# Kernel tuning notes

Measured on AMD Instinct MI355X. Metric: run time of the kernel, lower is better.

The kernel has to match this reference:

```python
import jax, jax.numpy as jnp
import numpy as np

EMB = 64
N_LEFT = 100000   # m: rows of left_features, b
N_RIGHT = 100000  # n: rows of right_features, c
N_EDGES = 3200000


def setup_inputs() -> dict:
    key = jax.random.key(0)
    ks = jax.random.split(key, 12)
    inp = {
        "left_features": jax.random.normal(ks[0], (N_LEFT, EMB), jnp.float32),
        "right_features_k": jax.random.normal(ks[1], (N_RIGHT, EMB), jnp.float32),
        "edge_index": jax.random.randint(ks[2], (N_EDGES, 2), 0, N_RIGHT, jnp.int64),
        "edge_weight": jax.random.uniform(ks[3], (N_EDGES,), jnp.float32),
        "right_features": jax.random.normal(ks[4], (N_RIGHT, EMB), jnp.float32),
        "c": jax.random.normal(ks[5], (N_RIGHT, 1), jnp.float32),
        "b": jax.random.normal(ks[6], (N_LEFT, 1), jnp.float32),
        # learned parameters
        "temp": jnp.full((2,), 0.9, jnp.float32),
        "W1": jax.random.normal(ks[7], (EMB, EMB), jnp.float32) * 0.05,
        "b1": jnp.zeros((EMB,), jnp.float32),
        "W2": jax.random.normal(ks[8], (EMB, EMB), jnp.float32) * 0.05,
        "b2": jnp.zeros((EMB,), jnp.float32),
    }
    return inp


def reference(left_features, right_features_k, edge_index, edge_weight,
              right_features, c, b, temp, W1, b1, W2, b2):
    # right_to_left=False branch of BipartiteGraphConvolution.forward
    n = right_features.shape[0]  # = c.shape[0]
    # Source quirk: values.sum(dim=-1) on a 1-D vector is a GLOBAL scalar sum,
    # clamped to min 1; every edge weight is scaled by 1/that scalar.
    total = jnp.maximum(jnp.sum(edge_weight), 1.0)
    vals = edge_weight / total                                    # [E]
    row = edge_index[:, 0]  # destination (right) node, in [0, n)
    col = edge_index[:, 1]  # source (left) node, in [0, m)
    # sparse-dense matmul: conv_output = A @ left_features, A in COO (coalesce
    # just sums duplicate entries, identical to segment-sum over raw edges)
    msg = left_features[col] * vals[:, None]                      # [E, EMB]
    conv_output = jax.ops.segment_sum(msg, row, num_segments=n)   # [n, EMB]
    h = right_features + temp[1] * (c - conv_output)              # [n, EMB]
    # output_module: Linear -> ReLU -> Linear (torch Linear: x @ W.T + b)
    h = jax.nn.relu(h @ W1.T + b1)
    out = h @ W2.T + b2
    return out
```

## Files before the change

### kernel.cpp

```cpp
#include <hip/hip_runtime.h>

#define EMB 64
#define BROWS 512
#define BSHIFT 9
#define CHUNK2 2048
#define COLBITS 23
#define COLMASK ((1u << COLBITS) - 1u)
#define MROWS 64
#define HPAD 66

__device__ __forceinline__ unsigned short f2bf(float f) {
    unsigned u = __float_as_uint(f);
    u = u + 0x7FFFu + ((u >> 16) & 1u);
    return (unsigned short)(u >> 16);
}

__global__ void convert_left_kernel(const float* __restrict__ left,
                                    unsigned* __restrict__ left16, int n2) {
    int i = blockIdx.x * blockDim.x + threadIdx.x;
    if (i >= n2) return;
    float2 v = ((const float2*)left)[i];
    left16[i] = (unsigned)f2bf(v.x) | ((unsigned)f2bf(v.y) << 16);
}

__global__ void init_bcur_kernel(int* __restrict__ bcur, int nb, int slot) {
    int t = threadIdx.x;
    if (t < nb) bcur[t] = t * slot;
}

__global__ __launch_bounds__(256) void partition2_kernel(
    const int2* __restrict__ eidx, const float* __restrict__ w, int n_edges,
    int nb, int* __restrict__ bcursor, int2* __restrict__ bsorted,
    float* __restrict__ total) {
    __shared__ int lcur[256];
    __shared__ int go[256];
    int t = threadIdx.x;
    int base = blockIdx.x * CHUNK2;

    lcur[t] = 0;
    __syncthreads();

    int2 pay[8];
    int bb[8];
    int rr[8];
    float s = 0.f;
    #pragma unroll
    for (int k = 0; k < 8; ++k) {
        int e = base + t + k * 256;
        if (e < n_edges) {
            int2 rc = eidx[e];
            float wv = w[e];
            s += wv;
            int b = rc.x >> BSHIFT;
            pay[k] = make_int2(
                (int)(((unsigned)(rc.x & (BROWS - 1)) << COLBITS) |
                      (unsigned)rc.y),
                __float_as_int(wv));
            bb[k] = b;
            rr[k] = atomicAdd(&lcur[b], 1);
        } else {
            bb[k] = -1;
        }
    }
    #pragma unroll
    for (int off = 32; off > 0; off >>= 1) s += __shfl_down(s, off, 64);
    if ((t & 63) == 0) atomicAdd(total, s);
    __syncthreads();

    if (t < nb) {
        int v = lcur[t];
        go[t] = (v > 0) ? atomicAdd(&bcursor[t], v) : 0;
    }
    __syncthreads();

    #pragma unroll
    for (int k = 0; k < 8; ++k) {
        if (bb[k] >= 0) bsorted[(size_t)go[bb[k]] + rr[k]] = pay[k];
    }
}

__global__ __launch_bounds__(256, 1) void count_scan_kernel(
    const int* __restrict__ bcur, int* __restrict__ sbase, int nb, int slot) {
    __shared__ int ssc[256];
    int t = threadIdx.x;
    int cnt = (t < nb) ? (bcur[t] - t * slot) : 0;
    ssc[t] = cnt;
    __syncthreads();
    for (int off = 1; off < 256; off <<= 1) {
        int u = (t >= off) ? ssc[t - off] : 0;
        __syncthreads();
        ssc[t] += u;
        __syncthreads();
    }
    if (t < nb) sbase[t] = ssc[t] - cnt;
}

__global__ __launch_bounds__(1024) void local_rowsort_kernel(
    const int2* __restrict__ bsorted, const int* __restrict__ bcur,
    const int* __restrict__ sbase, int* __restrict__ offs,
    int2* __restrict__ sorted2, int n_right, int slot) {
    __shared__ int lhist[BROWS];
    __shared__ int lcur[BROWS];
    __shared__ int ps[BROWS];
    int b = blockIdx.x;
    int t = threadIdx.x;
    int src0 = b * slot;
    int send = min(bcur[b], src0 + slot);
    int dbase = sbase[b];
    int row0 = b << BSHIFT;
    int nrows = min(BROWS, n_right - row0);

    if (t < BROWS) lhist[t] = 0;
    __syncthreads();
    for (int e = src0 + t; e < send; e += 1024)
        atomicAdd(&lhist[((unsigned)bsorted[e].x) >> COLBITS], 1);
    __syncthreads();

    if (t < BROWS) ps[t] = lhist[t];
    __syncthreads();
    for (int off = 1; off < BROWS; off <<= 1) {
        int u = (t < BROWS && t >= off) ? ps[t - off] : 0;
        __syncthreads();
        if (t < BROWS) ps[t] += u;
        __syncthreads();
    }
    if (t < BROWS) {
        int excl = ps[t] - lhist[t];
        lcur[t] = excl;
        if (t < nrows) offs[row0 + t] = dbase + excl;
    }
    __syncthreads();

    int e = src0 + t;
    for (; e + 3 * 1024 < send; e += 4 * 1024) {
        int2 e0 = bsorted[e + 0 * 1024];
        int2 e1 = bsorted[e + 1 * 1024];
        int2 e2 = bsorted[e + 2 * 1024];
        int2 e3 = bsorted[e + 3 * 1024];
        int p0 = atomicAdd(&lcur[((unsigned)e0.x) >> COLBITS], 1);
        int p1 = atomicAdd(&lcur[((unsigned)e1.x) >> COLBITS], 1);
        int p2 = atomicAdd(&lcur[((unsigned)e2.x) >> COLBITS], 1);
        int p3 = atomicAdd(&lcur[((unsigned)e3.x) >> COLBITS], 1);
        sorted2[dbase + p0] = e0;
        sorted2[dbase + p1] = e1;
        sorted2[dbase + p2] = e2;
        sorted2[dbase + p3] = e3;
    }
    for (; e < send; e += 1024) {
        int2 e0 = bsorted[e];
        int p0 = atomicAdd(&lcur[((unsigned)e0.x) >> COLBITS], 1);
        sorted2[dbase + p0] = e0;
    }
}

__global__ void seg_gather_bf16_kernel(const int2* __restrict__ sorted,
                                       const int* __restrict__ offs,
                                       const uint4* __restrict__ left16o,
                                       const float* __restrict__ right,
                                       const float* __restrict__ c,
                                       const float* __restrict__ temp,
                                       const float* __restrict__ total,
                                       float* __restrict__ hout, int n_right,
                                       int n_edges, int offs_are_ends) {
    int gid = blockIdx.x * blockDim.x + threadIdx.x;
    int wid = gid >> 6;
    int lane = gid & 63;
    if (wid >= n_right) return;
    int start, end;
    if (offs_are_ends) {
        end = offs[wid];
        start = (wid == 0) ? 0 : offs[wid - 1];
    } else {
        start = offs[wid];
        end = (wid + 1 < n_right) ? offs[wid + 1] : n_edges;
    }

    int sub = lane >> 3;
    int d8  = lane & 7;

    float cv = c[wid];
    float inv = 1.0f / fmaxf(total[0], 1.0f);
    float t1 = temp[1];

    float a0 = 0.f, a1 = 0.f, a2 = 0.f, a3 = 0.f;
    float a4 = 0.f, a5 = 0.f, a6 = 0.f, a7 = 0.f;

    if (start < end) {
        int ee = start + sub;
        int2 sv = sorted[(ee < end) ? ee : (end - 1)];
        for (int base = start; base < end; base += 8) {
            int2 cur = sv;
            int ecur = base + sub;
            int bnext = base + 8;
            if (bnext < end) {
                int en = bnext + sub;
                sv = sorted[(en < end) ? en : (end - 1)];
            }
            float wv = (ecur < end) ? __int_as_float(cur.y) : 0.f;
            unsigned col = (unsigned)cur.x & COLMASK;
            uint4 pk = left16o[(size_t)col * 8 + d8];
            a0 = fmaf(wv, __uint_as_float(pk.x << 16), a0);
            a1 = fmaf(wv, __uint_as_float(pk.x & 0xffff0000u), a1);
            a2 = fmaf(wv, __uint_as_float(pk.y << 16), a2);
            a3 = fmaf(wv, __uint_as_float(pk.y & 0xffff0000u), a3);
            a4 = fmaf(wv, __uint_as_float(pk.z << 16), a4);
            a5 = fmaf(wv, __uint_as_float(pk.z & 0xffff0000u), a5);
            a6 = fmaf(wv, __uint_as_float(pk.w << 16), a6);
            a7 = fmaf(wv, __uint_as_float(pk.w & 0xffff0000u), a7);
        }
    }

    #define RED8(x) x += __shfl_xor(x, 8, 64); x += __shfl_xor(x, 16, 64); \
                    x += __shfl_xor(x, 32, 64);
    RED8(a0) RED8(a1) RED8(a2) RED8(a3) RED8(a4) RED8(a5) RED8(a6) RED8(a7)
    #undef RED8

    if (lane < 8) {
        const float4* rp = (const float4*)(right + (size_t)wid * EMB);
        float4 r0 = rp[2 * lane];
        float4 r1 = rp[2 * lane + 1];
        float4 h0, h1;
        h0.x = r0.x + t1 * (cv - a0 * inv);
        h0.y = r0.y + t1 * (cv - a1 * inv);
        h0.z = r0.z + t1 * (cv - a2 * inv);
        h0.w = r0.w + t1 * (cv - a3 * inv);
        h1.x = r1.x + t1 * (cv - a4 * inv);
        h1.y = r1.y + t1 * (cv - a5 * inv);
        h1.z = r1.z + t1 * (cv - a6 * inv);
        h1.w = r1.w + t1 * (cv - a7 * inv);
        float4* op = (float4*)(hout + (size_t)wid * EMB);
        op[2 * lane] = h0;
        op[2 * lane + 1] = h1;
    }
}

__global__ __launch_bounds__(256, 4) void mlp_kernel(
    const float* __restrict__ W1, const float* __restrict__ b1,
    const float* __restrict__ W2, const float* __restrict__ b2,
    float* __restrict__ io, int n) {
    __shared__ float hT[64 * HPAD];
    __shared__ float h1T[64 * 64];
    int t = threadIdx.x;
    int r = t & 63;
    int q = __builtin_amdgcn_readfirstlane(t >> 6);
    int row0 = blockIdx.x * MROWS;

    #pragma unroll
    for (int i = 0; i < 16; ++i) {
        int rr = i * 4 + q;
        int gr = row0 + rr;
        float v = (gr < n) ? io[(size_t)gr * EMB + r] : 0.f;
        hT[r * HPAD + rr] = v;
    }
    __syncthreads();

    float acc[16];
    #pragma unroll
    for (int jj = 0; jj < 16; ++jj) acc[jj] = b1[q * 16 + jj];
    for (int k = 0; k < 64; ++k) {
        float hk = hT[k * HPAD + r];
        #pragma unroll
        for (int jj = 0; jj < 16; ++jj)
            acc[jj] = fmaf(hk, W1[(q * 16 + jj) * EMB + k], acc[jj]);
    }
    #pragma unroll
    for (int jj = 0; jj < 16; ++jj)
        h1T[(q * 16 + jj) * 64 + r] = fmaxf(acc[jj], 0.f);
    __syncthreads();

    #pragma unroll
    for (int jj = 0; jj < 16; ++jj) acc[jj] = b2[q * 16 + jj];
    for (int k = 0; k < 64; ++k) {
        float hk = h1T[k * 64 + r];
        #pragma unroll
        for (int jj = 0; jj < 16; ++jj)
            acc[jj] = fmaf(hk, W2[(q * 16 + jj) * EMB + k], acc[jj]);
    }
    __syncthreads();
    #pragma unroll
    for (int jj = 0; jj < 16; ++jj)
        hT[(q * 16 + jj) * HPAD + r] = acc[jj];
    __syncthreads();

    #pragma unroll
    for (int i = 0; i < 16; ++i) {
        int rr = i * 4 + q;
        int gr = row0 + rr;
        if (gr < n) io[(size_t)gr * EMB + r] = hT[r * HPAD + rr];
    }
}


__global__ void hist_total_kernel(const int2* __restrict__ eidx,
                                  const float* __restrict__ w, int n_edges,
                                  int* __restrict__ counts,
                                  float* __restrict__ total) {
    int gid = blockIdx.x * blockDim.x + threadIdx.x;
    int stride = gridDim.x * blockDim.x;
    float s = 0.f;
    for (int e = gid; e < n_edges; e += stride) {
        s += w[e];
        atomicAdd(&counts[eidx[e].x], 1);
    }
    #pragma unroll
    for (int off = 32; off > 0; off >>= 1) s += __shfl_down(s, off, 64);
    if ((threadIdx.x & 63) == 0) atomicAdd(total, s);
}

__global__ __launch_bounds__(1024, 1) void scan1_kernel(
    const int* __restrict__ cnt, int* __restrict__ incl,
    int* __restrict__ bsums, int n) {
    __shared__ int s[1024];
    int t = threadIdx.x;
    int i = blockIdx.x * 1024 + t;
    int v = (i < n) ? cnt[i] : 0;
    s[t] = v;
    __syncthreads();
    for (int off = 1; off < 1024; off <<= 1) {
        int u = (t >= off) ? s[t - off] : 0;
        __syncthreads();
        s[t] += u;
        __syncthreads();
    }
    if (i < n) incl[i] = s[t];
    if (t == 1023) bsums[blockIdx.x] = s[t];
}

__global__ __launch_bounds__(256, 1) void scan2_kernel(int* __restrict__ bsums, int nb) {
    __shared__ int s[256];
    int t = threadIdx.x;
    int v = (t < nb) ? bsums[t] : 0;
    s[t] = v;
    __syncthreads();
    for (int off = 1; off < 256; off <<= 1) {
        int u = (t >= off) ? s[t - off] : 0;
        __syncthreads();
        s[t] += u;
        __syncthreads();
    }
    if (t < nb) bsums[t] = s[t] - v;
}

__global__ void scan3_kernel(const int* __restrict__ incl,
                             const int* __restrict__ base,
                             int* __restrict__ offs, int n) {
    int i = blockIdx.x * blockDim.x + threadIdx.x;
    if (i >= n) return;
    offs[i] = (i == 0) ? 0 : incl[i - 1] + base[(i - 1) >> 10];
}

__global__ void scatter_kernel(const int2* __restrict__ eidx,
                               const float* __restrict__ w, int n_edges,
                               int* __restrict__ offs,
                               int2* __restrict__ sorted) {
    int gid = blockIdx.x * blockDim.x + threadIdx.x;
    int stride = gridDim.x * blockDim.x;
    for (int e = gid; e < n_edges; e += stride) {
        int2 rc = eidx[e];
        float v = w[e];
        int pos = atomicAdd(&offs[rc.x], 1);
        sorted[pos] = make_int2(rc.y, __float_as_int(v));
    }
}


__global__ void sum_weights_kernel(const float* __restrict__ w, int n,
                                   float* __restrict__ total) {
    int gid = blockIdx.x * blockDim.x + threadIdx.x;
    int stride = gridDim.x * blockDim.x;
    float s = 0.f;
    for (int i = gid; i < n; i += stride) s += w[i];
    #pragma unroll
    for (int off = 32; off > 0; off >>= 1) s += __shfl_down(s, off, 64);
    if ((threadIdx.x & 63) == 0) atomicAdd(total, s);
}

__global__ void edge_scatter_kernel(const int* __restrict__ idx,
                                    const float* __restrict__ w,
                                    const float* __restrict__ left,
                                    const float* __restrict__ total,
                                    float* __restrict__ conv,
                                    long long n_threads) {
    long long gid = (long long)blockIdx.x * blockDim.x + threadIdx.x;
    if (gid >= n_threads) return;
    int e = (int)(gid >> 6);
    int d = (int)(gid & 63);
    float inv = 1.0f / fmaxf(total[0], 1.0f);
    int row = idx[2 * e];
    int col = idx[2 * e + 1];
    float v = w[e] * inv;
    float msg = left[(size_t)col * EMB + d] * v;
    atomicAdd(&conv[(size_t)row * EMB + d], msg);
}

__global__ __launch_bounds__(256, 1) void fused_mlp_kernel(
    const float* __restrict__ right, const float* __restrict__ c,
    const float* __restrict__ temp,
    const float* __restrict__ W1, const float* __restrict__ b1,
    const float* __restrict__ W2, const float* __restrict__ b2,
    float* __restrict__ io, int n) {
    int r = blockIdx.x * blockDim.x + threadIdx.x;
    if (r >= n) return;
    float t1 = temp[1];
    float cv = c[r];
    float h[EMB];
    const float4* rp = (const float4*)(right + (size_t)r * EMB);
    const float4* qp = (const float4*)(io + (size_t)r * EMB);
    #pragma unroll
    for (int qq = 0; qq < EMB / 4; ++qq) {
        float4 rv = rp[qq];
        float4 qv = qp[qq];
        h[4 * qq + 0] = rv.x + t1 * (cv - qv.x);
        h[4 * qq + 1] = rv.y + t1 * (cv - qv.y);
        h[4 * qq + 2] = rv.z + t1 * (cv - qv.z);
        h[4 * qq + 3] = rv.w + t1 * (cv - qv.w);
    }
    float h1[EMB];
    #pragma unroll
    for (int j = 0; j < EMB; j += 4) {
        float s0 = b1[j], s1 = b1[j + 1], s2 = b1[j + 2], s3 = b1[j + 3];
        #pragma unroll
        for (int k = 0; k < EMB; ++k) {
            float hk = h[k];
            s0 = fmaf(hk, W1[(j + 0) * EMB + k], s0);
            s1 = fmaf(hk, W1[(j + 1) * EMB + k], s1);
            s2 = fmaf(hk, W1[(j + 2) * EMB + k], s2);
            s3 = fmaf(hk, W1[(j + 3) * EMB + k], s3);
        }
        h1[j] = fmaxf(s0, 0.f);
        h1[j + 1] = fmaxf(s1, 0.f);
        h1[j + 2] = fmaxf(s2, 0.f);
        h1[j + 3] = fmaxf(s3, 0.f);
    }
    float4* op = (float4*)(io + (size_t)r * EMB);
    #pragma unroll
    for (int j = 0; j < EMB; j += 4) {
        float s0 = b2[j], s1 = b2[j + 1], s2 = b2[j + 2], s3 = b2[j + 3];
        #pragma unroll
        for (int k = 0; k < EMB; ++k) {
            float hk = h1[k];
            s0 = fmaf(hk, W2[(j + 0) * EMB + k], s0);
            s1 = fmaf(hk, W2[(j + 1) * EMB + k], s1);
            s2 = fmaf(hk, W2[(j + 2) * EMB + k], s2);
            s3 = fmaf(hk, W2[(j + 3) * EMB + k], s3);
        }
        op[j / 4] = make_float4(s0, s1, s2, s3);
    }
}


extern "C" void kernel_launch(void* const* d_in, const int* in_sizes, int n_in,
                              void* d_out, int out_size, void* d_ws, size_t ws_size,
                              hipStream_t stream) {
    const float* left   = (const float*)d_in[0];
    const int*   eidx   = (const int*)d_in[2];
    const float* ew     = (const float*)d_in[3];
    const float* right  = (const float*)d_in[4];
    const float* c      = (const float*)d_in[5];
    const float* temp   = (const float*)d_in[7];
    const float* W1     = (const float*)d_in[8];
    const float* b1     = (const float*)d_in[9];
    const float* W2     = (const float*)d_in[10];
    const float* b2     = (const float*)d_in[11];

    const int n_edges = in_sizes[3];
    const int n_right = in_sizes[4] / EMB;
    const int n_left  = in_sizes[0] / EMB;
    float* out = (float*)d_out;

    const int nb = (n_right + BROWS - 1) >> BSHIFT;
    const int nblocks_scan = (n_right + 1023) / 1024;

    auto align256 = [](size_t x) { return (x + 255) & ~(size_t)255; };

    int slot = n_edges / (nb > 0 ? nb : 1);
    slot += slot / 16 + 128;

    size_t off_bcur    = 64;
    size_t off_sbase   = align256(off_bcur + (size_t)nb * 4);
    size_t off_offs    = align256(off_sbase + (size_t)(nb + 1) * 4);
    size_t off_bsorted = align256(off_offs + (size_t)n_right * 4);
    size_t off_sorted2 = align256(off_bsorted + ((size_t)nb * slot + slot) * 8);
    size_t off_left16f = align256(off_sorted2 + (size_t)n_edges * 8);
    size_t req_full    = off_left16f + (size_t)n_left * EMB * 2;

    size_t m_off_offs   = 64;
    size_t m_off_incl   = align256(m_off_offs + (size_t)n_right * 4);
    size_t m_off_bsum   = align256(m_off_incl + (size_t)n_right * 4);
    size_t m_off_sorted = align256(m_off_bsum + 1024);
    size_t m_off_left16 = align256(m_off_sorted + (size_t)n_edges * 8);
    size_t req_mid      = m_off_left16 + (size_t)n_left * EMB * 2;

    bool common_ok = (nb <= 256) && (nblocks_scan <= 256) &&
                     (n_left <= (1 << COLBITS)) && (BROWS * nb >= n_right);

    if (common_ok && ws_size >= req_full) {
        char* ws = (char*)d_ws;
        float* total = (float*)ws;
        int* bcur = (int*)(ws + off_bcur);
        int* sbase = (int*)(ws + off_sbase);
        int* offs = (int*)(ws + off_offs);
        int2* bsorted = (int2*)(ws + off_bsorted);
        int2* sorted2 = (int2*)(ws + off_sorted2);
        unsigned short* left16 = (unsigned short*)(ws + off_left16f);

        hipMemsetAsync(ws, 0, 64, stream);

        int n2 = n_left * EMB / 2;
        convert_left_kernel<<<(n2 + 255) / 256, 256, 0, stream>>>(
            left, (unsigned*)left16, n2);
        init_bcur_kernel<<<1, 256, 0, stream>>>(bcur, nb, slot);
        {
            int nchunks = (n_edges + CHUNK2 - 1) / CHUNK2;
            partition2_kernel<<<nchunks, 256, 0, stream>>>(
                (const int2*)eidx, ew, n_edges, nb, bcur, bsorted, total);
        }
        count_scan_kernel<<<1, 256, 0, stream>>>(bcur, sbase, nb, slot);
        local_rowsort_kernel<<<nb, 1024, 0, stream>>>(bsorted, bcur, sbase, offs,
                                                      sorted2, n_right, slot);
        {
            long long n_threads = (long long)n_right * EMB;
            int blocks = (int)((n_threads + 255) / 256);
            seg_gather_bf16_kernel<<<blocks, 256, 0, stream>>>(
                sorted2, offs, (const uint4*)left16, right, c, temp, total,
                out, n_right, n_edges, 0);
        }
        mlp_kernel<<<(n_right + MROWS - 1) / MROWS, 256, 0, stream>>>(
            W1, b1, W2, b2, out, n_right);
    } else if (common_ok && ws_size >= req_mid) {
        char* ws = (char*)d_ws;
        float* total = (float*)ws;
        int* offs = (int*)(ws + m_off_offs);
        int* incl = (int*)(ws + m_off_incl);
        int* bsum = (int*)(ws + m_off_bsum);
        int2* sorted = (int2*)(ws + m_off_sorted);
        unsigned short* left16 = (unsigned short*)(ws + m_off_left16);

        hipMemsetAsync(ws, 0, m_off_offs + (size_t)n_right * 4, stream);

        int n2 = n_left * EMB / 2;
        convert_left_kernel<<<(n2 + 255) / 256, 256, 0, stream>>>(
            left, (unsigned*)left16, n2);
        hist_total_kernel<<<2048, 256, 0, stream>>>((const int2*)eidx, ew,
                                                    n_edges, offs, total);
        scan1_kernel<<<nblocks_scan, 1024, 0, stream>>>(offs, incl, bsum, n_right);
        scan2_kernel<<<1, 256, 0, stream>>>(bsum, nblocks_scan);
        scan3_kernel<<<(n_right + 255) / 256, 256, 0, stream>>>(incl, bsum, offs,
                                                                n_right);
        scatter_kernel<<<2048, 256, 0, stream>>>((const int2*)eidx, ew, n_edges,
                                                 offs, sorted);
        {
            long long n_threads = (long long)n_right * EMB;
            int blocks = (int)((n_threads + 255) / 256);
            seg_gather_bf16_kernel<<<blocks, 256, 0, stream>>>(
                sorted, offs, (const uint4*)left16, right, c, temp, total,
                out, n_right, n_edges, 1);
        }
        mlp_kernel<<<(n_right + MROWS - 1) / MROWS, 256, 0, stream>>>(
            W1, b1, W2, b2, out, n_right);
    } else {
        float* total = (float*)d_ws;
        hipMemsetAsync(d_out, 0, (size_t)out_size * sizeof(float), stream);
        hipMemsetAsync(d_ws, 0, sizeof(float), stream);
        sum_weights_kernel<<<2048, 256, 0, stream>>>(ew, n_edges, total);
        long long n_threads = (long long)n_edges * EMB;
        long long blocks = (n_threads + 255) / 256;
        edge_scatter_kernel<<<(int)blocks, 256, 0, stream>>>(
            eidx, ew, left, total, out, n_threads);
        int mblocks = (n_right + 255) / 256;
        fused_mlp_kernel<<<mblocks, 256, 0, stream>>>(right, c, temp, W1, b1, W2,
                                                      b2, out, n_right);
    }
}
```

Before: 271.7 us.

## Stage bucket-partitioned edges in shared memory for coalesced scatter writes

The edge partition kernel now runs a per-block histogram pass and prefix scan first, reserves global bucket ranges up front, then stages edges in shared memory ordered by bucket. It writes them out in contiguous order so the global scatter becomes mostly coalesced runs. Chunk size doubles to 4096 with 1024-thread blocks. The cost is reading the edge indices twice, a 256-entry scan, and a larger shared-memory footprint that may limit occupancy.

```diff
diff --git a/kernel.cpp b/kernel.cpp
--- a/kernel.cpp
+++ b/kernel.cpp
@@ -3,7 +3,7 @@
 #define EMB 64
 #define BROWS 512
 #define BSHIFT 9
-#define CHUNK2 2048
+#define CHUNK 4096
 #define COLBITS 23
 #define COLMASK ((1u << COLBITS) - 1u)
 #define MROWS 64
@@ -28,54 +28,69 @@
     if (t < nb) bcur[t] = t * slot;
 }
 
-__global__ __launch_bounds__(256) void partition2_kernel(
+__global__ __launch_bounds__(1024, 8) void partition_kernel(
     const int2* __restrict__ eidx, const float* __restrict__ w, int n_edges,
-    int nb, int* __restrict__ bcursor, int2* __restrict__ bsorted,
+    int* __restrict__ bcursor, int2* __restrict__ bsorted,
     float* __restrict__ total) {
+    __shared__ int lh[256];
+    __shared__ int lo[256];
+    __shared__ int go[256];
     __shared__ int lcur[256];
-    __shared__ int go[256];
-    int t = threadIdx.x;
-    int base = blockIdx.x * CHUNK2;
-
-    lcur[t] = 0;
-    __syncthreads();
-
-    int2 pay[8];
-    int bb[8];
-    int rr[8];
+    __shared__ int2 stage[CHUNK];
+    __shared__ int dstg[CHUNK];
+    int t = threadIdx.x;
+    int base = blockIdx.x * CHUNK;
+    int cnt = min(CHUNK, n_edges - base);
+
+    if (t < 256) lh[t] = 0;
+    __syncthreads();
+    #pragma unroll
+    for (int k = 0; k < CHUNK / 1024; ++k) {
+        int e = base + t + k * 1024;
+        if (e < n_edges) atomicAdd(&lh[eidx[e].x >> BSHIFT], 1);
+    }
+    __syncthreads();
+    int v = (t < 256) ? lh[t] : 0;
+    if (t < 256) lo[t] = v;
+    __syncthreads();
+    for (int off = 1; off < 256; off <<= 1) {
+        int u = (t < 256 && t >= off) ? lo[t - off] : 0;
+        __syncthreads();
+        if (t < 256) lo[t] += u;
+        __syncthreads();
+    }
+    if (t < 256) {
+        int excl = lo[t] - v;
+        go[t] = (v > 0) ? atomicAdd(&bcursor[t], v) : 0;
+        lo[t] = excl;
+        lcur[t] = excl;
+    }
+    __syncthreads();
+
     float s = 0.f;
     #pragma unroll
-    for (int k = 0; k < 8; ++k) {
-        int e = base + t + k * 256;
+    for (int k = 0; k < CHUNK / 1024; ++k) {
+        int e = base + t + k * 1024;
         if (e < n_edges) {
             int2 rc = eidx[e];
             float wv = w[e];
             s += wv;
             int b = rc.x >> BSHIFT;
-            pay[k] = make_int2(
-                (int)(((unsigned)(rc.x & (BROWS - 1)) << COLBITS) |
-                      (unsigned)rc.y),
-                __float_as_int(wv));
-            bb[k] = b;
-            rr[k] = atomicAdd(&lcur[b], 1);
-        } else {
-            bb[k] = -1;
+            unsigned rl = (unsigned)(rc.x & (BROWS - 1));
+            int p = atomicAdd(&lcur[b], 1);
+            stage[p] = make_int2((int)((rl << COLBITS) | (unsigned)rc.y),
+                                 __float_as_int(wv));
+            dstg[p] = go[b] + (p - lo[b]);
         }
     }
     #pragma unroll
     for (int off = 32; off > 0; off >>= 1) s += __shfl_down(s, off, 64);
     if ((t & 63) == 0) atomicAdd(total, s);
     __syncthreads();
-
-    if (t < nb) {
-        int v = lcur[t];
-        go[t] = (v > 0) ? atomicAdd(&bcursor[t], v) : 0;
-    }
-    __syncthreads();
-
-    #pragma unroll
-    for (int k = 0; k < 8; ++k) {
-        if (bb[k] >= 0) bsorted[(size_t)go[bb[k]] + rr[k]] = pay[k];
+    #pragma unroll
+    for (int k = 0; k < CHUNK / 1024; ++k) {
+        int s2 = t + k * 1024;
+        if (s2 < cnt) bsorted[dstg[s2]] = stage[s2];
     }
 }
 
@@ -511,9 +526,9 @@
             left, (unsigned*)left16, n2);
         init_bcur_kernel<<<1, 256, 0, stream>>>(bcur, nb, slot);
         {
-            int nchunks = (n_edges + CHUNK2 - 1) / CHUNK2;
-            partition2_kernel<<<nchunks, 256, 0, stream>>>(
-                (const int2*)eidx, ew, n_edges, nb, bcur, bsorted, total);
+            int nchunks = (n_edges + CHUNK - 1) / CHUNK;
+            partition_kernel<<<nchunks, 1024, 0, stream>>>(
+                (const int2*)eidx, ew, n_edges, bcur, bsorted, total);
         }
         count_scan_kernel<<<1, 256, 0, stream>>>(bcur, sbase, nb, slot);
         local_rowsort_kernel<<<nb, 1024, 0, stream>>>(bsorted, bcur, sbase, offs,
```

Measured after the change: 341.4 us. 25.6% more time.
